# Optimization experiments

Measured on AMD Instinct MI355X. Metric: run time of the kernel, lower is better.

The kernel has to match this reference:

```python
import jax, jax.numpy as jnp
import numpy as np

B, S, T, E, H = 16, 96, 50, 128, 128
D2 = 2 * H
V = 32000
NGRAM = 2
ALPHA = 0.25


def _lstm(x, Wih, Whh, b, reverse=False):
    # x: [N, T, E] -> outputs [N, T, H], final h, c (PyTorch gate order i,f,g,o)
    xt = jnp.swapaxes(x, 0, 1)
    if reverse:
        xt = xt[::-1]
    n = x.shape[0]
    h = Whh.shape[1]
    init = (jnp.zeros((n, h), x.dtype), jnp.zeros((n, h), x.dtype))

    def step(carry, xin):
        hprev, cprev = carry
        g = xin @ Wih.T + hprev @ Whh.T + b
        i, f, gg, o = jnp.split(g, 4, axis=-1)
        c = jax.nn.sigmoid(f) * cprev + jax.nn.sigmoid(i) * jnp.tanh(gg)
        hnew = jax.nn.sigmoid(o) * jnp.tanh(c)
        return (hnew, c), hnew

    (hT, cT), outs = jax.lax.scan(step, init, xt)
    if reverse:
        outs = outs[::-1]
    return jnp.swapaxes(outs, 0, 1), hT, cT


def _gru(x, h, Wi, Wh, bi, bh):
    # PyTorch GRUCell, gate order r,z,n
    gi = x @ Wi.T + bi
    gh = h @ Wh.T + bh
    ir, iz, inn = jnp.split(gi, 3, axis=-1)
    hr, hz, hn = jnp.split(gh, 3, axis=-1)
    r = jax.nn.sigmoid(ir + hr)
    z = jax.nn.sigmoid(iz + hz)
    n = jnp.tanh(inn + r * hn)
    return (1.0 - z) * n + z * h


def _norm_scale(x):
    # (||x|| + alpha) / (||x|| + 1), detached as in the original
    v = jnp.linalg.norm(x, axis=1)
    return jax.lax.stop_gradient(((v + ALPHA) / (v + 1.0))[:, None])


def setup_inputs() -> dict:
    key = jax.random.key(0)
    ks = jax.random.split(key, 30)
    rn = lambda k, sh: jax.random.normal(k, sh, jnp.float32) * 0.05
    return {
        "enc_batch": jax.random.randint(ks[0], (B * S, T), 0, V),
        "struct_parent": jax.random.randint(ks[1], (B, S, S), 0, B * S + 1),
        "struct_child": jax.random.randint(ks[2], (B, S, S), 0, B * S + 1),
        "mask_emb": (jax.random.uniform(ks[3], (B, S, S, 1)) < 0.2).astype(jnp.float32),
        "emb_table": rn(ks[4], (V, E)),
        "Wih_f": rn(ks[5], (4 * H, E)), "Whh_f": rn(ks[6], (4 * H, H)), "b_f": rn(ks[7], (4 * H,)),
        "Wih_b": rn(ks[8], (4 * H, E)), "Whh_b": rn(ks[9], (4 * H, H)), "b_b": rn(ks[10], (4 * H,)),
        "Wc": rn(ks[11], (H, D2)), "bc": rn(ks[12], (H,)),
        "Whr": rn(ks[13], (H, D2)), "bhr": rn(ks[14], (H,)),
        "Wi_cp": rn(ks[15], (3 * D2, D2)), "Wh_cp": rn(ks[16], (3 * D2, D2)),
        "bi_cp": rn(ks[17], (3 * D2,)), "bh_cp": rn(ks[18], (3 * D2,)),
        "Wi_pc": rn(ks[19], (3 * D2, D2)), "Wh_pc": rn(ks[20], (3 * D2, D2)),
        "bi_pc": rn(ks[21], (3 * D2,)), "bh_pc": rn(ks[22], (3 * D2,)),
    }


def reference(enc_batch, struct_parent, struct_child, mask_emb, emb_table,
              Wih_f, Whh_f, b_f, Wih_b, Whh_b, b_b, Wc, bc, Whr, bhr,
              Wi_cp, Wh_cp, bi_cp, bh_cp, Wi_pc, Wh_pc, bi_pc, bh_pc):
    # Sentence encoder (bidirectional LSTM); dropout=0 -> identity
    emb = emb_table[enc_batch]                       # [B*S, T, E]
    _, hf, cf = _lstm(emb, Wih_f, Whh_f, b_f)
    _, hb, cb = _lstm(emb, Wih_b, Whh_b, b_b, reverse=True)
    c_red = jax.nn.relu(jnp.concatenate([cf, cb], 1) @ Wc.T + bc)
    h_red = jax.nn.relu(jnp.concatenate([hf, hb], 1) @ Whr.T + bhr)
    enc_states = jnp.concatenate([c_red, h_red], 1)  # [B*S, 2H]
    zero = jnp.zeros((1, D2), enc_states.dtype)
    hidden = jnp.concatenate([zero, enc_states], 0)  # [B*S+1, 2H]; row 0 = zero_emb

    # child -> parent message passing
    for _ in range(NGRAM):
        p = hidden[struct_parent].reshape(-1, D2)    # gather [B*S*S, 2H]
        c = hidden[struct_child].reshape(-1, D2)
        ch = _gru(c, p, Wi_cp, Wh_cp, bi_cp, bh_cp).reshape(B, S, S, D2)
        ch = (ch * mask_emb).sum(1).reshape(B * S, D2)
        ch = jnp.concatenate([zero, ch], 0)
        hidden = hidden + ch * _norm_scale(ch)

    # parent -> child message passing
    for _ in range(NGRAM):
        p = hidden[struct_parent].reshape(-1, D2)
        c = hidden[struct_child].reshape(-1, D2)
        ch = _gru(p, c, Wi_pc, Wh_pc, bi_pc, bh_pc).reshape(B, S, S, D2)
        ch = (ch * mask_emb).sum(2).reshape(B * S, D2)
        ch = jnp.concatenate([zero, ch], 0)
        hidden = hidden + ch * _norm_scale(ch)

    return hidden
```

## Files before the change

kernel.cpp:

```cpp
#include <hip/hip_runtime.h>

typedef unsigned short u16;
typedef __attribute__((ext_vector_type(8))) short bf8;
typedef __attribute__((ext_vector_type(4))) short s16x4;
typedef __attribute__((ext_vector_type(4))) float f32x4;
typedef __attribute__((ext_vector_type(4))) int   i32x4;
typedef __attribute__((ext_vector_type(2))) int   i32x2;

#define S_   96
#define T_   50
#define NSEQ 1536
#define NR   1537
#define XROW 520

__device__ __forceinline__ float bf2f(u16 u){ return __uint_as_float(((unsigned)u)<<16); }
__device__ __forceinline__ u16 f2bf(float f){
  unsigned u = __float_as_uint(f);
  u += 0x7fffu + ((u>>16)&1u);
  return (u16)(u>>16);
}
__device__ __forceinline__ int cvtpk(float lo, float hi){
  int r; asm("v_cvt_pk_bf16_f32 %0, %1, %2" : "=v"(r) : "v"(lo), "v"(hi)); return r;
}
__device__ __forceinline__ float sigm(float x){
  return __builtin_amdgcn_rcpf(1.f + __expf(-x));
}
__device__ __forceinline__ float tanh_(float x){
  return 1.f - 2.f*__builtin_amdgcn_rcpf(__expf(2.f*x) + 1.f);
}
__device__ __forceinline__ void bar_lds(){
  asm volatile("s_waitcnt lgkmcnt(0)\n\ts_barrier" ::: "memory");
}

struct CvtArgs { const float* s[10]; u16* d[10]; };
__global__ __launch_bounds__(256) void prep_kernel(CvtArgs a,
    const int* __restrict__ par, const int* __restrict__ chi,
    const float* __restrict__ mask,
    int2* __restrict__ ent0, int* __restrict__ cnt0,
    int2* __restrict__ ent1, int* __restrict__ cnt1)
{
  if (blockIdx.x < 1088){
    int e = (blockIdx.x*256 + threadIdx.x)*4;
    if (e >= 1114112) return;
    int t, off;
    if (e < 262144){ t = e>>16; off = e & 65535; }
    else if (e < 327680){ int e2=e-262144; t = 4+(e2>>15); off = e2&32767; }
    else { int e3=e-327680; t = 6 + e3/196608; off = e3%196608; }
    int src = off;
    if (t < 4){
      int colp = off>>7, k = off&127;
      int orig = ((colp>>4)&3)*128 + ((colp>>6)<<4) + (colp&15);
      src = orig*128 + k;
    }
    f32x4 v = *reinterpret_cast<const f32x4*>(a.s[t]+src);
    i32x2 o;
    o[0] = cvtpk(v[0], v[1]);
    o[1] = cvtpk(v[2], v[3]);
    *reinterpret_cast<i32x2*>(a.d[t]+off) = o;
  } else {
    const int rr = blockIdx.x - 1088;
    __shared__ int c0s, c1s;
    if (threadIdx.x==0){ c0s=0; c1s=0; }
    __syncthreads();
    const int l = threadIdx.x;
    if (l < S_){
      const int b = rr/S_, fx = rr%S_, base = b*S_*S_;
      int idx = base + l*S_ + fx;
      if (mask[idx] != 0.f){
        int p = atomicAdd(&c0s, 1);
        ent0[rr*S_ + p] = make_int2(chi[idx], par[idx]);
      }
      int jdx = base + fx*S_ + l;
      if (mask[jdx] != 0.f){
        int p = atomicAdd(&c1s, 1);
        ent1[rr*S_ + p] = make_int2(par[jdx], chi[jdx]);
      }
    }
    __syncthreads();
    if (threadIdx.x==0){ cnt0[rr]=c0s; cnt1[rr]=c1s; }
  }
}

__global__ __launch_bounds__(512, 2) void lstm_kernel(
    const int* __restrict__ enc, const float* __restrict__ emb,
    const u16* __restrict__ WihF, const u16* __restrict__ WhhF, const float* __restrict__ bF,
    const u16* __restrict__ WihB, const u16* __restrict__ WhhB, const float* __restrict__ bB,
    u16* __restrict__ c_cat, u16* __restrict__ h_cat)
{
  __shared__ short xh[16*XROW];
  __shared__ int   toks[16*T_];

  const int tid  = threadIdx.x;
  const int wave = tid>>6;
  const int lane = tid&63;
  const int dir  = blockIdx.y;
  const int s0   = blockIdx.x*16;

  const u16* Wih = dir ? WihB : WihF;
  const u16* Whh = dir ? WhhB : WhhF;
  const float* bb = dir ? bB  : bF;

  for (int i=tid; i<16*T_; i+=512)
    toks[i] = enc[(s0 + i/T_)*T_ + (i%T_)];

  const int mL   = lane&15;
  const int quad = lane>>4;
  const int kb   = quad*8;

  bf8 Breg[4][8];
  f32x4 bias4[4];
  #pragma unroll
  for (int n=0;n<4;n++){
    int colp = wave*64 + n*16 + mL;
    bias4[n] = *reinterpret_cast<const f32x4*>(bb + n*128 + wave*16 + quad*4);
    #pragma unroll
    for (int ks=0;ks<8;ks++){
      int k = ks*32 + kb;
      const u16* p = (k<128) ? (Wih + colp*128 + k) : (Whh + colp*128 + (k-128));
      Breg[n][ks] = *reinterpret_cast<const bf8*>(p);
      asm volatile("" : "+v"(Breg[n][ks]));
    }
  }

  if (tid<256){
    int r = tid>>4, c = tid&15;
    *reinterpret_cast<i32x4*>(&xh[r*XROW + 256 + c*8]) = (i32x4){0,0,0,0};
  }

  const int srow = tid>>5, schunk = tid&31;
  float cst[4] = {0.f,0.f,0.f,0.f};
  float hst[4] = {0.f,0.f,0.f,0.f};

  __syncthreads();

  {
    int tok0 = toks[srow*T_ + (dir ? (T_-1) : 0)];
    f32x4 x0 = *reinterpret_cast<const f32x4*>(emb + tok0*128 + schunk*4);
    int tok1 = toks[srow*T_ + (dir ? (T_-2) : 1)];
    f32x4 x1 = *reinterpret_cast<const f32x4*>(emb + tok1*128 + schunk*4);
    i32x2 p0; p0[0]=cvtpk(x0[0],x0[1]); p0[1]=cvtpk(x0[2],x0[3]);
    i32x2 p1; p1[0]=cvtpk(x1[0],x1[1]); p1[1]=cvtpk(x1[2],x1[3]);
    *reinterpret_cast<i32x2*>(&xh[srow*XROW +       schunk*4]) = p0;
    *reinterpret_cast<i32x2*>(&xh[srow*XROW + 128 + schunk*4]) = p1;
  }
  f32x4 xvA, xvB;
  {
    int tA = toks[srow*T_ + (dir ? (T_-3) : 2)];
    xvA = *reinterpret_cast<const f32x4*>(emb + tA*128 + schunk*4);
    int tB = toks[srow*T_ + (dir ? (T_-4) : 3)];
    xvB = *reinterpret_cast<const f32x4*>(emb + tB*128 + schunk*4);
  }
  __syncthreads();

  f32x4 accx[4];
  #pragma unroll
  for (int n=0;n<4;n++) accx[n] = (f32x4){0.f,0.f,0.f,0.f};
  #pragma unroll
  for (int ks=0;ks<4;ks++){
    bf8 b = *reinterpret_cast<const bf8*>(&xh[mL*XROW + ks*32 + kb]);
    #pragma unroll
    for (int n=0;n<4;n++)
      accx[n] = __builtin_amdgcn_mfma_f32_16x16x32_bf16(Breg[n][ks], b, accx[n], 0,0,0);
  }
  bar_lds();

  for (int t=0;t<T_;t++){
    const int cb = t&1, nb = cb^1;

    f32x4 acc[4];
    #pragma unroll
    for (int n=0;n<4;n++) acc[n] = accx[n];
    #pragma unroll
    for (int ks=0;ks<4;ks++){
      bf8 b = *reinterpret_cast<const bf8*>(&xh[mL*XROW + 256 + cb*128 + ks*32 + kb]);
      #pragma unroll
      for (int n=0;n<4;n++)
        acc[n] = __builtin_amdgcn_mfma_f32_16x16x32_bf16(Breg[n][4+ks], b, acc[n], 0,0,0);
    }

    if (t+2 < T_){
      i32x2 p; p[0]=cvtpk(xvA[0],xvA[1]); p[1]=cvtpk(xvA[2],xvA[3]);
      *reinterpret_cast<i32x2*>(&xh[srow*XROW + cb*128 + schunk*4]) = p;
    }
    xvA = xvB;
    if (t+4 < T_){
      int tok = toks[srow*T_ + (dir ? (T_-5-t) : (t+4))];
      xvB = *reinterpret_cast<const f32x4*>(emb + tok*128 + schunk*4);
    }

    if (t+1 < T_){
      #pragma unroll
      for (int n=0;n<4;n++) accx[n] = (f32x4){0.f,0.f,0.f,0.f};
      #pragma unroll
      for (int ks=0;ks<4;ks++){
        bf8 b = *reinterpret_cast<const bf8*>(&xh[mL*XROW + nb*128 + ks*32 + kb]);
        #pragma unroll
        for (int n=0;n<4;n++)
          accx[n] = __builtin_amdgcn_mfma_f32_16x16x32_bf16(Breg[n][ks], b, accx[n], 0,0,0);
      }
    }

    float hv4[4];
    #pragma unroll
    for (int i=0;i<4;i++){
      float gi_ = acc[0][i]+bias4[0][i];
      float gf_ = acc[1][i]+bias4[1][i];
      float gg_ = acc[2][i]+bias4[2][i];
      float go_ = acc[3][i]+bias4[3][i];
      float c = sigm(gf_)*cst[i] + sigm(gi_)*tanh_(gg_);
      float h = sigm(go_)*tanh_(c);
      cst[i]=c; hst[i]=h; hv4[i]=h;
    }
    i32x2 hp;
    hp[0]=cvtpk(hv4[0],hv4[1]); hp[1]=cvtpk(hv4[2],hv4[3]);
    *reinterpret_cast<i32x2*>(&xh[mL*XROW + 256 + nb*128 + wave*16 + quad*4]) = hp;
    bar_lds();
  }

  {
    const int ch = wave*16 + quad*4;
    const int gs = s0 + mL;
    i32x2 cp_, hp_;
    cp_[0]=cvtpk(cst[0],cst[1]); cp_[1]=cvtpk(cst[2],cst[3]);
    hp_[0]=cvtpk(hst[0],hst[1]); hp_[1]=cvtpk(hst[2],hst[3]);
    *reinterpret_cast<i32x2*>(c_cat + gs*256 + dir*128 + ch) = cp_;
    *reinterpret_cast<i32x2*>(h_cat + gs*256 + dir*128 + ch) = hp_;
  }
}

__global__ __launch_bounds__(256) void reduce_kernel(
    const u16* __restrict__ c_cat, const u16* __restrict__ h_cat,
    const u16* __restrict__ Wc, const float* __restrict__ bc,
    const u16* __restrict__ Whr, const float* __restrict__ bhr,
    float* __restrict__ hidf, u16* __restrict__ hidb)
{
  const int tid=threadIdx.x, wave=tid>>6, lane=tid&63;
  const int mL=lane&15, quad=lane>>4, kb=quad*8;
  const int m0 = blockIdx.x*64;
  const u16* A    = (wave<2) ? c_cat : h_cat;
  const u16* W    = (wave<2) ? Wc  : Whr;
  const float* bv = (wave<2) ? bc  : bhr;
  const int nb    = (wave&1)*64;
  const int obase = (wave<2) ? 0 : 128;

  f32x4 acc[4][4];
  #pragma unroll
  for (int mt=0;mt<4;mt++)
    #pragma unroll
    for (int nt=0;nt<4;nt++) acc[mt][nt] = (f32x4){0.f,0.f,0.f,0.f};

  #pragma unroll
  for (int ks=0;ks<8;ks++){
    int k = ks*32 + kb;
    bf8 bfr[4];
    #pragma unroll
    for (int nt=0;nt<4;nt++)
      bfr[nt] = *reinterpret_cast<const bf8*>(W + (nb+nt*16+mL)*256 + k);
    #pragma unroll
    for (int mt=0;mt<4;mt++){
      bf8 a = *reinterpret_cast<const bf8*>(A + (m0+mt*16+mL)*256 + k);
      #pragma unroll
      for (int nt=0;nt<4;nt++)
        acc[mt][nt] = __builtin_amdgcn_mfma_f32_16x16x32_bf16(a, bfr[nt], acc[mt][nt], 0,0,0);
    }
  }
  const int row0 = quad*4;
  float biasv[4];
  #pragma unroll
  for (int nt=0;nt<4;nt++) biasv[nt] = bv[nb+nt*16+mL];
  #pragma unroll
  for (int mt=0;mt<4;mt++){
    #pragma unroll
    for (int nt=0;nt<4;nt++){
      int col = obase + nb + nt*16 + mL;
      #pragma unroll
      for (int i=0;i<4;i++){
        int r = m0 + mt*16 + row0 + i;
        float v = fmaxf(acc[mt][nt][i] + biasv[nt], 0.f);
        hidf[(r+1)*256 + col] = v;
        hidb[(r+1)*256 + col] = f2bf(v);
      }
    }
  }
  if (blockIdx.x==0 && tid<64){
    #pragma unroll
    for (int j=0;j<4;j++){ hidf[tid*4+j] = 0.f; hidb[tid*4+j] = 0; }
  }
}

__global__ __launch_bounds__(256) void gates_gemm_kernel(
    const u16* __restrict__ hidb,
    const u16* __restrict__ Wi, const u16* __restrict__ Wh,
    const float* __restrict__ bi, const float* __restrict__ bh,
    u16* __restrict__ gi, u16* __restrict__ gh)
{
  const int tid=threadIdx.x, wave=tid>>6, lane=tid&63;
  const int mL=lane&15, quad=lane>>4, kb=quad*8;
  const int m0 = blockIdx.x*32;
  const int n0 = blockIdx.y*128 + wave*32;
  const bool isI = (n0 < 768);
  const u16* W    = isI ? Wi : Wh;
  const float* bv = isI ? bi : bh;
  u16* out        = isI ? gi : gh;
  const int nbc   = isI ? n0 : (n0-768);

  int arow[2];
  #pragma unroll
  for (int mt=0;mt<2;mt++) arow[mt] = min(m0+mt*16+mL, NR-1);

  f32x4 acc[2][2];
  #pragma unroll
  for (int mt=0;mt<2;mt++)
    #pragma unroll
    for (int nt=0;nt<2;nt++) acc[mt][nt] = (f32x4){0.f,0.f,0.f,0.f};

  #pragma unroll
  for (int ks=0;ks<8;ks++){
    int k = ks*32 + kb;
    bf8 bfr[2];
    #pragma unroll
    for (int nt=0;nt<2;nt++)
      bfr[nt] = *reinterpret_cast<const bf8*>(W + (nbc+nt*16+mL)*256 + k);
    #pragma unroll
    for (int mt=0;mt<2;mt++){
      bf8 a = *reinterpret_cast<const bf8*>(hidb + arow[mt]*256 + k);
      #pragma unroll
      for (int nt=0;nt<2;nt++)
        acc[mt][nt] = __builtin_amdgcn_mfma_f32_16x16x32_bf16(a, bfr[nt], acc[mt][nt], 0,0,0);
    }
  }
  const int row0 = quad*4;
  float biasv[2];
  #pragma unroll
  for (int nt=0;nt<2;nt++) biasv[nt] = bv[nbc+nt*16+mL];
  #pragma unroll
  for (int mt=0;mt<2;mt++){
    #pragma unroll
    for (int nt=0;nt<2;nt++){
      #pragma unroll
      for (int i=0;i<4;i++){
        int r = m0 + mt*16 + row0 + i;
        if (r < NR)
          out[r*768 + nbc + nt*16 + mL] = f2bf(acc[mt][nt][i] + biasv[nt]);
      }
    }
  }
}

__global__ __launch_bounds__(512) void pair_kernel(
    const u16* __restrict__ gi, const u16* __restrict__ gh,
    const float* __restrict__ hin,
    float* __restrict__ hout, u16* __restrict__ bout, float* __restrict__ dout,
    const int2* __restrict__ ent, const int* __restrict__ cnt)
{
  const int r = blockIdx.x;
  const int tid = threadIdx.x, wave = tid>>6, lane = tid&63;
  __shared__ float part[8][260];
  __shared__ float ssum[4];
  if (r==0){
    if (tid<256){
      hout[tid]=0.f; bout[tid]=0;
      if (dout) dout[tid]=0.f;
    }
    return;
  }
  const int rr = r-1;
  const int n  = cnt[rr];
  const int2* e = ent + rr*S_;
  const int ch0 = lane*4;

  float a0=0.f, a1=0.f, a2=0.f, a3=0.f;
  for (int k=wave; k<n; k+=8){
    int2 pr = e[k];
    const u16* gx = gi + pr.x*768 + ch0;
    const u16* gy = gh + pr.y*768 + ch0;
    s16x4 vi0 = *reinterpret_cast<const s16x4*>(gx);
    s16x4 vi1 = *reinterpret_cast<const s16x4*>(gx+256);
    s16x4 vi2 = *reinterpret_cast<const s16x4*>(gx+512);
    s16x4 vh0 = *reinterpret_cast<const s16x4*>(gy);
    s16x4 vh1 = *reinterpret_cast<const s16x4*>(gy+256);
    s16x4 vh2 = *reinterpret_cast<const s16x4*>(gy+512);
    f32x4 hv  = *reinterpret_cast<const f32x4*>(hin + pr.y*256 + ch0);
    float o[4];
    #pragma unroll
    for (int i=0;i<4;i++){
      float rg = sigm(bf2f((u16)vi0[i]) + bf2f((u16)vh0[i]));
      float zg = sigm(bf2f((u16)vi1[i]) + bf2f((u16)vh1[i]));
      float ng = tanh_(bf2f((u16)vi2[i]) + rg*bf2f((u16)vh2[i]));
      o[i] = (1.f-zg)*ng + zg*hv[i];
    }
    a0 += o[0]; a1 += o[1]; a2 += o[2]; a3 += o[3];
  }
  *reinterpret_cast<f32x4*>(&part[wave][ch0]) = (f32x4){a0,a1,a2,a3};
  __syncthreads();

  if (tid < 256){
    float tot = part[0][tid] + part[1][tid] + part[2][tid] + part[3][tid]
              + part[4][tid] + part[5][tid] + part[6][tid] + part[7][tid];
    part[0][tid] = tot;
    float sq = tot*tot;
    #pragma unroll
    for (int off=32; off>0; off>>=1) sq += __shfl_xor(sq, off, 64);
    if (lane==0) ssum[wave] = sq;
  }
  __syncthreads();
  if (tid < 256){
    float tot = part[0][tid];
    float v  = sqrtf(ssum[0]+ssum[1]+ssum[2]+ssum[3]);
    float sc = (v + 0.25f)*__builtin_amdgcn_rcpf(v + 1.f);
    float nv = hin[r*256 + tid] + tot*sc;
    hout[r*256 + tid] = nv;
    bout[r*256 + tid] = f2bf(nv);
    if (dout) dout[r*256 + tid] = nv;
  }
}

extern "C" void kernel_launch(void* const* d_in, const int* in_sizes, int n_in,
                              void* d_out, int out_size, void* d_ws, size_t ws_size,
                              hipStream_t stream)
{
  const int*   enc  = (const int*)  d_in[0];
  const int*   spar = (const int*)  d_in[1];
  const int*   schi = (const int*)  d_in[2];
  const float* mask = (const float*)d_in[3];
  const float* emb  = (const float*)d_in[4];
  const float* WihF = (const float*)d_in[5];
  const float* WhhF = (const float*)d_in[6];
  const float* bF   = (const float*)d_in[7];
  const float* WihB = (const float*)d_in[8];
  const float* WhhB = (const float*)d_in[9];
  const float* bB   = (const float*)d_in[10];
  const float* Wc   = (const float*)d_in[11];
  const float* bc   = (const float*)d_in[12];
  const float* Whr  = (const float*)d_in[13];
  const float* bhr  = (const float*)d_in[14];
  const float* WiCP = (const float*)d_in[15];
  const float* WhCP = (const float*)d_in[16];
  const float* biCP = (const float*)d_in[17];
  const float* bhCP = (const float*)d_in[18];
  const float* WiPC = (const float*)d_in[19];
  const float* WhPC = (const float*)d_in[20];
  const float* biPC = (const float*)d_in[21];
  const float* bhPC = (const float*)d_in[22];

  char* ws = (char*)d_ws;
  u16*   c_cat = (u16*)  (ws + 0);
  u16*   h_cat = (u16*)  (ws + 786432);
  float* hf0   = (float*)(ws + 1572864);
  float* hf1   = (float*)(ws + 3146752);
  u16*   hb    = (u16*)  (ws + 4720640);
  u16*   gi    = (u16*)  (ws + 5507584);
  u16*   gh    = (u16*)  (ws + 7868416);
  u16*   wbf   = (u16*)  (ws + 10229248);
  int2*  ent0  = (int2*) (ws + 12457472);
  int2*  ent1  = (int2*) (ws + 13637120);
  int*   cnt0  = (int*)  (ws + 14816768);
  int*   cnt1  = (int*)  (ws + 14822912);
  float* out   = (float*)d_out;

  u16* bWihF = wbf + 0;
  u16* bWhhF = wbf + 65536;
  u16* bWihB = wbf + 131072;
  u16* bWhhB = wbf + 196608;
  u16* bWc   = wbf + 262144;
  u16* bWhr  = wbf + 294912;
  u16* bWiCP = wbf + 327680;
  u16* bWhCP = wbf + 524288;
  u16* bWiPC = wbf + 720896;
  u16* bWhPC = wbf + 917504;

  CvtArgs ca;
  ca.s[0]=WihF; ca.s[1]=WhhF; ca.s[2]=WihB; ca.s[3]=WhhB;
  ca.s[4]=Wc;   ca.s[5]=Whr;
  ca.s[6]=WiCP; ca.s[7]=WhCP; ca.s[8]=WiPC; ca.s[9]=WhPC;
  ca.d[0]=bWihF; ca.d[1]=bWhhF; ca.d[2]=bWihB; ca.d[3]=bWhhB;
  ca.d[4]=bWc;   ca.d[5]=bWhr;
  ca.d[6]=bWiCP; ca.d[7]=bWhCP; ca.d[8]=bWiPC; ca.d[9]=bWhPC;
  prep_kernel<<<dim3(1088+NSEQ), dim3(256), 0, stream>>>(
      ca, spar, schi, mask, ent0, cnt0, ent1, cnt1);

  lstm_kernel<<<dim3(96,2), dim3(512), 0, stream>>>(
      enc, emb, bWihF,bWhhF,bF, bWihB,bWhhB,bB, c_cat, h_cat);
  reduce_kernel<<<dim3(24), dim3(256), 0, stream>>>(
      c_cat,h_cat, bWc,bc,bWhr,bhr, hf0,hb);

  float* hfb[2] = {hf0,hf1};
  int cur = 0;
  for (int it=0; it<4; it++){
    const u16* Wi   = (it<2)?bWiCP:bWiPC;
    const u16* Wh   = (it<2)?bWhCP:bWhPC;
    const float* bi = (it<2)?biCP:biPC;
    const float* bh = (it<2)?bhCP:bhPC;
    int nxt = cur^1;
    gates_gemm_kernel<<<dim3(49,12), dim3(256), 0, stream>>>(
        hb, Wi,Wh,bi,bh, gi,gh);
    pair_kernel<<<dim3(NR), dim3(512), 0, stream>>>(
        gi,gh, hfb[cur], hfb[nxt], hb,
        (it==3)?out:(float*)nullptr,
        (it<2)?ent0:ent1, (it<2)?cnt0:cnt1);
    cur = nxt;
  }
}
```

Baseline: 316.8 us.

## Fuse reduce, gate GEMMs and pair passes into one persistent kernel with grid barriers

```diff
diff --git a/kernel.cpp b/kernel.cpp
--- a/kernel.cpp
+++ b/kernel.cpp
@@ -12,6 +12,7 @@
 #define NSEQ 1536
 #define NR   1537
 #define XROW 520
+#define FGRID 512
 
 __device__ __forceinline__ float bf2f(u16 u){ return __uint_as_float(((unsigned)u)<<16); }
 __device__ __forceinline__ u16 f2bf(float f){
@@ -31,15 +32,27 @@
 __device__ __forceinline__ void bar_lds(){
   asm volatile("s_waitcnt lgkmcnt(0)\n\ts_barrier" ::: "memory");
 }
+__device__ __forceinline__ void gsync(unsigned* bar){
+  __syncthreads();
+  if (threadIdx.x == 0){
+    unsigned t = __hip_atomic_fetch_add(bar, 1u, __ATOMIC_ACQ_REL, __HIP_MEMORY_SCOPE_AGENT);
+    unsigned target = (t/FGRID + 1u)*FGRID;
+    while (__hip_atomic_load(bar, __ATOMIC_ACQUIRE, __HIP_MEMORY_SCOPE_AGENT) < target)
+      __builtin_amdgcn_s_sleep(8);
+  }
+  __syncthreads();
+}
 
 struct CvtArgs { const float* s[10]; u16* d[10]; };
 __global__ __launch_bounds__(256) void prep_kernel(CvtArgs a,
     const int* __restrict__ par, const int* __restrict__ chi,
     const float* __restrict__ mask,
     int2* __restrict__ ent0, int* __restrict__ cnt0,
-    int2* __restrict__ ent1, int* __restrict__ cnt1)
+    int2* __restrict__ ent1, int* __restrict__ cnt1,
+    unsigned* __restrict__ bar)
 {
   if (blockIdx.x < 1088){
+    if (blockIdx.x==0 && threadIdx.x==0) *bar = 0u;
     int e = (blockIdx.x*256 + threadIdx.x)*4;
     if (e >= 1114112) return;
     int t, off;
@@ -228,190 +241,212 @@
   }
 }
 
-__global__ __launch_bounds__(256) void reduce_kernel(
+__global__ __launch_bounds__(512, 4) void fused_kernel(
     const u16* __restrict__ c_cat, const u16* __restrict__ h_cat,
-    const u16* __restrict__ Wc, const float* __restrict__ bc,
+    const u16* __restrict__ Wc,  const float* __restrict__ bc,
     const u16* __restrict__ Whr, const float* __restrict__ bhr,
-    float* __restrict__ hidf, u16* __restrict__ hidb)
+    float* __restrict__ hf0, float* __restrict__ hf1, u16* __restrict__ hb,
+    const u16* __restrict__ WiCP, const u16* __restrict__ WhCP,
+    const float* __restrict__ biCP, const float* __restrict__ bhCP,
+    const u16* __restrict__ WiPC, const u16* __restrict__ WhPC,
+    const float* __restrict__ biPC, const float* __restrict__ bhPC,
+    u16* __restrict__ gi, u16* __restrict__ gh,
+    const int2* __restrict__ ent0, const int* __restrict__ cnt0,
+    const int2* __restrict__ ent1, const int* __restrict__ cnt1,
+    float* __restrict__ out, unsigned* __restrict__ bar)
 {
-  const int tid=threadIdx.x, wave=tid>>6, lane=tid&63;
-  const int mL=lane&15, quad=lane>>4, kb=quad*8;
-  const int m0 = blockIdx.x*64;
-  const u16* A    = (wave<2) ? c_cat : h_cat;
-  const u16* W    = (wave<2) ? Wc  : Whr;
-  const float* bv = (wave<2) ? bc  : bhr;
-  const int nb    = (wave&1)*64;
-  const int obase = (wave<2) ? 0 : 128;
-
-  f32x4 acc[4][4];
-  #pragma unroll
-  for (int mt=0;mt<4;mt++)
-    #pragma unroll
-    for (int nt=0;nt<4;nt++) acc[mt][nt] = (f32x4){0.f,0.f,0.f,0.f};
-
-  #pragma unroll
-  for (int ks=0;ks<8;ks++){
-    int k = ks*32 + kb;
-    bf8 bfr[4];
-    #pragma unroll
-    for (int nt=0;nt<4;nt++)
-      bfr[nt] = *reinterpret_cast<const bf8*>(W + (nb+nt*16+mL)*256 + k);
-    #pragma unroll
-    for (int mt=0;mt<4;mt++){
-      bf8 a = *reinterpret_cast<const bf8*>(A + (m0+mt*16+mL)*256 + k);
-      #pragma unroll
-      for (int nt=0;nt<4;nt++)
-        acc[mt][nt] = __builtin_amdgcn_mfma_f32_16x16x32_bf16(a, bfr[nt], acc[mt][nt], 0,0,0);
-    }
-  }
-  const int row0 = quad*4;
-  float biasv[4];
-  #pragma unroll
-  for (int nt=0;nt<4;nt++) biasv[nt] = bv[nb+nt*16+mL];
-  #pragma unroll
-  for (int mt=0;mt<4;mt++){
-    #pragma unroll
-    for (int nt=0;nt<4;nt++){
-      int col = obase + nb + nt*16 + mL;
-      #pragma unroll
-      for (int i=0;i<4;i++){
-        int r = m0 + mt*16 + row0 + i;
-        float v = fmaxf(acc[mt][nt][i] + biasv[nt], 0.f);
-        hidf[(r+1)*256 + col] = v;
-        hidb[(r+1)*256 + col] = f2bf(v);
-      }
-    }
-  }
-  if (blockIdx.x==0 && tid<64){
-    #pragma unroll
-    for (int j=0;j<4;j++){ hidf[tid*4+j] = 0.f; hidb[tid*4+j] = 0; }
-  }
-}
-
-__global__ __launch_bounds__(256) void gates_gemm_kernel(
-    const u16* __restrict__ hidb,
-    const u16* __restrict__ Wi, const u16* __restrict__ Wh,
-    const float* __restrict__ bi, const float* __restrict__ bh,
-    u16* __restrict__ gi, u16* __restrict__ gh)
-{
-  const int tid=threadIdx.x, wave=tid>>6, lane=tid&63;
-  const int mL=lane&15, quad=lane>>4, kb=quad*8;
-  const int m0 = blockIdx.x*32;
-  const int n0 = blockIdx.y*128 + wave*32;
-  const bool isI = (n0 < 768);
-  const u16* W    = isI ? Wi : Wh;
-  const float* bv = isI ? bi : bh;
-  u16* out        = isI ? gi : gh;
-  const int nbc   = isI ? n0 : (n0-768);
-
-  int arow[2];
-  #pragma unroll
-  for (int mt=0;mt<2;mt++) arow[mt] = min(m0+mt*16+mL, NR-1);
-
-  f32x4 acc[2][2];
-  #pragma unroll
-  for (int mt=0;mt<2;mt++)
-    #pragma unroll
-    for (int nt=0;nt<2;nt++) acc[mt][nt] = (f32x4){0.f,0.f,0.f,0.f};
-
-  #pragma unroll
-  for (int ks=0;ks<8;ks++){
-    int k = ks*32 + kb;
-    bf8 bfr[2];
-    #pragma unroll
-    for (int nt=0;nt<2;nt++)
-      bfr[nt] = *reinterpret_cast<const bf8*>(W + (nbc+nt*16+mL)*256 + k);
-    #pragma unroll
-    for (int mt=0;mt<2;mt++){
-      bf8 a = *reinterpret_cast<const bf8*>(hidb + arow[mt]*256 + k);
-      #pragma unroll
-      for (int nt=0;nt<2;nt++)
-        acc[mt][nt] = __builtin_amdgcn_mfma_f32_16x16x32_bf16(a, bfr[nt], acc[mt][nt], 0,0,0);
-    }
-  }
-  const int row0 = quad*4;
-  float biasv[2];
-  #pragma unroll
-  for (int nt=0;nt<2;nt++) biasv[nt] = bv[nbc+nt*16+mL];
-  #pragma unroll
-  for (int mt=0;mt<2;mt++){
-    #pragma unroll
-    for (int nt=0;nt<2;nt++){
-      #pragma unroll
-      for (int i=0;i<4;i++){
-        int r = m0 + mt*16 + row0 + i;
-        if (r < NR)
-          out[r*768 + nbc + nt*16 + mL] = f2bf(acc[mt][nt][i] + biasv[nt]);
-      }
-    }
-  }
-}
-
-__global__ __launch_bounds__(512) void pair_kernel(
-    const u16* __restrict__ gi, const u16* __restrict__ gh,
-    const float* __restrict__ hin,
-    float* __restrict__ hout, u16* __restrict__ bout, float* __restrict__ dout,
-    const int2* __restrict__ ent, const int* __restrict__ cnt)
-{
-  const int r = blockIdx.x;
-  const int tid = threadIdx.x, wave = tid>>6, lane = tid&63;
   __shared__ float part[8][260];
   __shared__ float ssum[4];
-  if (r==0){
-    if (tid<256){
-      hout[tid]=0.f; bout[tid]=0;
-      if (dout) dout[tid]=0.f;
-    }
-    return;
-  }
-  const int rr = r-1;
-  const int n  = cnt[rr];
-  const int2* e = ent + rr*S_;
-  const int ch0 = lane*4;
-
-  float a0=0.f, a1=0.f, a2=0.f, a3=0.f;
-  for (int k=wave; k<n; k+=8){
-    int2 pr = e[k];
-    const u16* gx = gi + pr.x*768 + ch0;
-    const u16* gy = gh + pr.y*768 + ch0;
-    s16x4 vi0 = *reinterpret_cast<const s16x4*>(gx);
-    s16x4 vi1 = *reinterpret_cast<const s16x4*>(gx+256);
-    s16x4 vi2 = *reinterpret_cast<const s16x4*>(gx+512);
-    s16x4 vh0 = *reinterpret_cast<const s16x4*>(gy);
-    s16x4 vh1 = *reinterpret_cast<const s16x4*>(gy+256);
-    s16x4 vh2 = *reinterpret_cast<const s16x4*>(gy+512);
-    f32x4 hv  = *reinterpret_cast<const f32x4*>(hin + pr.y*256 + ch0);
-    float o[4];
-    #pragma unroll
-    for (int i=0;i<4;i++){
-      float rg = sigm(bf2f((u16)vi0[i]) + bf2f((u16)vh0[i]));
-      float zg = sigm(bf2f((u16)vi1[i]) + bf2f((u16)vh1[i]));
-      float ng = tanh_(bf2f((u16)vi2[i]) + rg*bf2f((u16)vh2[i]));
-      o[i] = (1.f-zg)*ng + zg*hv[i];
-    }
-    a0 += o[0]; a1 += o[1]; a2 += o[2]; a3 += o[3];
-  }
-  *reinterpret_cast<f32x4*>(&part[wave][ch0]) = (f32x4){a0,a1,a2,a3};
-  __syncthreads();
-
-  if (tid < 256){
-    float tot = part[0][tid] + part[1][tid] + part[2][tid] + part[3][tid]
-              + part[4][tid] + part[5][tid] + part[6][tid] + part[7][tid];
-    part[0][tid] = tot;
-    float sq = tot*tot;
-    #pragma unroll
-    for (int off=32; off>0; off>>=1) sq += __shfl_xor(sq, off, 64);
-    if (lane==0) ssum[wave] = sq;
-  }
-  __syncthreads();
-  if (tid < 256){
-    float tot = part[0][tid];
-    float v  = sqrtf(ssum[0]+ssum[1]+ssum[2]+ssum[3]);
-    float sc = (v + 0.25f)*__builtin_amdgcn_rcpf(v + 1.f);
-    float nv = hin[r*256 + tid] + tot*sc;
-    hout[r*256 + tid] = nv;
-    bout[r*256 + tid] = f2bf(nv);
-    if (dout) dout[r*256 + tid] = nv;
+
+  const int tid  = threadIdx.x;
+  const int half = tid>>8;
+  const int htid = tid&255;
+  const int hid  = blockIdx.x*2 + half;
+
+  if (hid < 24){
+    const int wave=htid>>6, lane=htid&63;
+    const int mL=lane&15, quad=lane>>4, kb=quad*8;
+    const int m0 = hid*64;
+    const u16* A    = (wave<2) ? c_cat : h_cat;
+    const u16* W    = (wave<2) ? Wc  : Whr;
+    const float* bv = (wave<2) ? bc  : bhr;
+    const int nb    = (wave&1)*64;
+    const int obase = (wave<2) ? 0 : 128;
+
+    f32x4 acc[4][4];
+    #pragma unroll
+    for (int mt=0;mt<4;mt++)
+      #pragma unroll
+      for (int nt=0;nt<4;nt++) acc[mt][nt] = (f32x4){0.f,0.f,0.f,0.f};
+
+    #pragma unroll
+    for (int ks=0;ks<8;ks++){
+      int k = ks*32 + kb;
+      bf8 bfr[4];
+      #pragma unroll
+      for (int nt=0;nt<4;nt++)
+        bfr[nt] = *reinterpret_cast<const bf8*>(W + (nb+nt*16+mL)*256 + k);
+      #pragma unroll
+      for (int mt=0;mt<4;mt++){
+        bf8 a = *reinterpret_cast<const bf8*>(A + (m0+mt*16+mL)*256 + k);
+        #pragma unroll
+        for (int nt=0;nt<4;nt++)
+          acc[mt][nt] = __builtin_amdgcn_mfma_f32_16x16x32_bf16(a, bfr[nt], acc[mt][nt], 0,0,0);
+      }
+    }
+    const int row0 = quad*4;
+    float biasv[4];
+    #pragma unroll
+    for (int nt=0;nt<4;nt++) biasv[nt] = bv[nb+nt*16+mL];
+    #pragma unroll
+    for (int mt=0;mt<4;mt++){
+      #pragma unroll
+      for (int nt=0;nt<4;nt++){
+        int col = obase + nb + nt*16 + mL;
+        #pragma unroll
+        for (int i=0;i<4;i++){
+          int r = m0 + mt*16 + row0 + i;
+          float v = fmaxf(acc[mt][nt][i] + biasv[nt], 0.f);
+          hf0[(r+1)*256 + col] = v;
+          hb[(r+1)*256 + col] = f2bf(v);
+        }
+      }
+    }
+    if (hid==0 && htid<64){
+      #pragma unroll
+      for (int j=0;j<4;j++){ hf0[htid*4+j] = 0.f; hb[htid*4+j] = 0; }
+    }
+  }
+  gsync(bar);
+
+  for (int it=0; it<4; ++it){
+    const u16* Wi   = (it<2)?WiCP:WiPC;
+    const u16* Wh   = (it<2)?WhCP:WhPC;
+    const float* bi = (it<2)?biCP:biPC;
+    const float* bh = (it<2)?bhCP:bhPC;
+
+    if (hid < 588){
+      const int wave=htid>>6, lane=htid&63;
+      const int mL=lane&15, quad=lane>>4, kb=quad*8;
+      const int m0 = (hid/12)*32;
+      const int n0 = (hid%12)*128 + wave*32;
+      const bool isI = (n0 < 768);
+      const u16* W    = isI ? Wi : Wh;
+      const float* bv = isI ? bi : bh;
+      u16* outp       = isI ? gi : gh;
+      const int nbc   = isI ? n0 : (n0-768);
+
+      int arow[2];
+      #pragma unroll
+      for (int mt=0;mt<2;mt++) arow[mt] = min(m0+mt*16+mL, NR-1);
+
+      f32x4 acc[2][2];
+      #pragma unroll
+      for (int mt=0;mt<2;mt++)
+        #pragma unroll
+        for (int nt=0;nt<2;nt++) acc[mt][nt] = (f32x4){0.f,0.f,0.f,0.f};
+
+      #pragma unroll
+      for (int ks=0;ks<8;ks++){
+        int k = ks*32 + kb;
+        bf8 bfr[2];
+        #pragma unroll
+        for (int nt=0;nt<2;nt++)
+          bfr[nt] = *reinterpret_cast<const bf8*>(W + (nbc+nt*16+mL)*256 + k);
+        #pragma unroll
+        for (int mt=0;mt<2;mt++){
+          bf8 a = *reinterpret_cast<const bf8*>(hb + arow[mt]*256 + k);
+          #pragma unroll
+          for (int nt=0;nt<2;nt++)
+            acc[mt][nt] = __builtin_amdgcn_mfma_f32_16x16x32_bf16(a, bfr[nt], acc[mt][nt], 0,0,0);
+        }
+      }
+      const int row0 = quad*4;
+      float biasv[2];
+      #pragma unroll
+      for (int nt=0;nt<2;nt++) biasv[nt] = bv[nbc+nt*16+mL];
+      #pragma unroll
+      for (int mt=0;mt<2;mt++){
+        #pragma unroll
+        for (int nt=0;nt<2;nt++){
+          #pragma unroll
+          for (int i=0;i<4;i++){
+            int r = m0 + mt*16 + row0 + i;
+            if (r < NR)
+              outp[r*768 + nbc + nt*16 + mL] = f2bf(acc[mt][nt][i] + biasv[nt]);
+          }
+        }
+      }
+    }
+    gsync(bar);
+
+    const int2* ent = (it<2)?ent0:ent1;
+    const int*  cnt = (it<2)?cnt0:cnt1;
+    const float* hin = (it&1)? hf1 : hf0;
+    float*       hout= (it&1)? hf0 : hf1;
+    float*       dout= (it==3)? out : (float*)nullptr;
+
+    for (int r=blockIdx.x; r<NR; r+=FGRID){
+      const int wave = tid>>6, lane = tid&63;
+      if (r==0){
+        if (tid<256){
+          hout[tid]=0.f; hb[tid]=0;
+          if (dout) dout[tid]=0.f;
+        }
+      } else {
+        const int rr = r-1;
+        const int n  = cnt[rr];
+        const int2* e = ent + rr*S_;
+        const int ch0 = lane*4;
+
+        float a0=0.f, a1=0.f, a2=0.f, a3=0.f;
+        for (int k=wave; k<n; k+=8){
+          int2 pr = e[k];
+          const u16* gx = gi + pr.x*768 + ch0;
+          const u16* gy = gh + pr.y*768 + ch0;
+          s16x4 vi0 = *reinterpret_cast<const s16x4*>(gx);
+          s16x4 vi1 = *reinterpret_cast<const s16x4*>(gx+256);
+          s16x4 vi2 = *reinterpret_cast<const s16x4*>(gx+512);
+          s16x4 vh0 = *reinterpret_cast<const s16x4*>(gy);
+          s16x4 vh1 = *reinterpret_cast<const s16x4*>(gy+256);
+          s16x4 vh2 = *reinterpret_cast<const s16x4*>(gy+512);
+          f32x4 hv  = *reinterpret_cast<const f32x4*>(hin + pr.y*256 + ch0);
+          float o[4];
+          #pragma unroll
+          for (int i=0;i<4;i++){
+            float rg = sigm(bf2f((u16)vi0[i]) + bf2f((u16)vh0[i]));
+            float zg = sigm(bf2f((u16)vi1[i]) + bf2f((u16)vh1[i]));
+            float ng = tanh_(bf2f((u16)vi2[i]) + rg*bf2f((u16)vh2[i]));
+            o[i] = (1.f-zg)*ng + zg*hv[i];
+          }
+          a0 += o[0]; a1 += o[1]; a2 += o[2]; a3 += o[3];
+        }
+        *reinterpret_cast<f32x4*>(&part[wave][ch0]) = (f32x4){a0,a1,a2,a3};
+        __syncthreads();
+
+        if (tid < 256){
+          float tot = part[0][tid] + part[1][tid] + part[2][tid] + part[3][tid]
+                    + part[4][tid] + part[5][tid] + part[6][tid] + part[7][tid];
+          part[0][tid] = tot;
+          float sq = tot*tot;
+          #pragma unroll
+          for (int off=32; off>0; off>>=1) sq += __shfl_xor(sq, off, 64);
+          if (lane==0) ssum[wave] = sq;
+        }
+        __syncthreads();
+        if (tid < 256){
+          float tot = part[0][tid];
+          float v  = sqrtf(ssum[0]+ssum[1]+ssum[2]+ssum[3]);
+          float sc = (v + 0.25f)*__builtin_amdgcn_rcpf(v + 1.f);
+          float nv = hin[r*256 + tid] + tot*sc;
+          hout[r*256 + tid] = nv;
+          hb[r*256 + tid] = f2bf(nv);
+          if (dout) dout[r*256 + tid] = nv;
+        }
+        __syncthreads();
+      }
+    }
+    gsync(bar);
   }
 }
 
@@ -456,6 +491,7 @@
   int2*  ent1  = (int2*) (ws + 13637120);
   int*   cnt0  = (int*)  (ws + 14816768);
   int*   cnt1  = (int*)  (ws + 14822912);
+  unsigned* bar= (unsigned*)(ws + 14829056);
   float* out   = (float*)d_out;
 
   u16* bWihF = wbf + 0;
@@ -477,27 +513,13 @@
   ca.d[4]=bWc;   ca.d[5]=bWhr;
   ca.d[6]=bWiCP; ca.d[7]=bWhCP; ca.d[8]=bWiPC; ca.d[9]=bWhPC;
   prep_kernel<<<dim3(1088+NSEQ), dim3(256), 0, stream>>>(
-      ca, spar, schi, mask, ent0, cnt0, ent1, cnt1);
+      ca, spar, schi, mask, ent0, cnt0, ent1, cnt1, bar);
 
   lstm_kernel<<<dim3(96,2), dim3(512), 0, stream>>>(
       enc, emb, bWihF,bWhhF,bF, bWihB,bWhhB,bB, c_cat, h_cat);
-  reduce_kernel<<<dim3(24), dim3(256), 0, stream>>>(
-      c_cat,h_cat, bWc,bc,bWhr,bhr, hf0,hb);
-
-  float* hfb[2] = {hf0,hf1};
-  int cur = 0;
-  for (int it=0; it<4; it++){
-    const u16* Wi   = (it<2)?bWiCP:bWiPC;
-    const u16* Wh   = (it<2)?bWhCP:bWhPC;
-    const float* bi = (it<2)?biCP:biPC;
-    const float* bh = (it<2)?bhCP:bhPC;
-    int nxt = cur^1;
-    gates_gemm_kernel<<<dim3(49,12), dim3(256), 0, stream>>>(
-        hb, Wi,Wh,bi,bh, gi,gh);
-    pair_kernel<<<dim3(NR), dim3(512), 0, stream>>>(
-        gi,gh, hfb[cur], hfb[nxt], hb,
-        (it==3)?out:(float*)nullptr,
-        (it<2)?ent0:ent1, (it<2)?cnt0:cnt1);
-    cur = nxt;
-  }
-}
+
+  fused_kernel<<<dim3(FGRID), dim3(512), 0, stream>>>(
+      c_cat, h_cat, bWc, bc, bWhr, bhr, hf0, hf1, hb,
+      bWiCP, bWhCP, biCP, bhCP, bWiPC, bWhPC, biPC, bhPC,
+      gi, gh, ent0, cnt0, ent1, cnt1, out, bar);
+}
```

New measurement: 1.159 ms. 266% more time.
